# Optimization experiments

Measured on AMD Instinct MI355X. Metric: run time of the kernel, lower is better.

The kernel has to match this reference:

```python
import jax, jax.numpy as jnp
import numpy as np

# GPT-2 decoder (mlm=False path of the Keras GPT module), no past/KV-cache,
# no explicit mask -> causal mask, dropout disabled (training=False).
N_HEAD = 12
NINF = -10000.0  # Attention.ninf
EPS = 1e-6


def layer_norm(x, g, b):
    m = jnp.mean(x, axis=-1, keepdims=True)
    v = jnp.mean(jnp.square(x - m), axis=-1, keepdims=True)
    return (x - m) / jnp.sqrt(v + EPS) * g + b


def gelu(x):
    # 0.5*x*(1+erf(x/sqrt(2))) as in gelu_activating
    return 0.5 * x * (1.0 + jax.lax.erf(x * np.float32(1.0 / np.sqrt(2.0))))


def setup_inputs() -> dict:
    key = jax.random.key(0)
    B, S, D, L, V, CTX = 4, 512, 768, 12, 50257, 1024
    F = 4 * D
    ks = jax.random.split(key, 10)
    init = lambda k, shape: (jax.random.normal(k, shape, jnp.float32) * 0.02)
    return {
        "x": jax.random.randint(ks[0], (B, S), 0, V),
        "emb": init(ks[1], (V, D)),        # wte (tied output projection)
        "posemb": init(ks[2], (CTX, D)),   # wpe
        "ln1_g": jnp.ones((L, D)), "ln1_b": jnp.zeros((L, D)),
        "wqkv": init(ks[3], (L, D, 3 * D)), "bqkv": jnp.zeros((L, 3 * D)),
        "wo": init(ks[4], (L, D, D)), "bo": jnp.zeros((L, D)),
        "ln2_g": jnp.ones((L, D)), "ln2_b": jnp.zeros((L, D)),
        "wfc": init(ks[5], (L, D, F)), "bfc": jnp.zeros((L, F)),
        "wproj": init(ks[6], (L, F, D)), "bproj": jnp.zeros((L, D)),
        "lnf_g": jnp.ones((D,)), "lnf_b": jnp.zeros((D,)),
    }


def reference(x, emb, posemb, ln1_g, ln1_b, wqkv, bqkv, wo, bo,
              ln2_g, ln2_b, wfc, bfc, wproj, bproj, lnf_g, lnf_b):
    B, S = x.shape
    L, D, _ = wqkv.shape
    H = N_HEAD
    hd = D // H
    scale = np.float32(1.0 / np.sqrt(hd))

    # Embedding (mlm=False): token + positional, no layernorm
    h = emb[x] + posemb[:S]  # [B,S,D]

    # causal mask: positions j > i get NINF (m1 = range(q)[:,None] < range(k)-k+q)
    mask = (jnp.arange(S)[:, None] < jnp.arange(S)[None, :]).astype(jnp.float32) * NINF

    for i in range(L):
        # pre-norm attention
        qkv = layer_norm(h, ln1_g[i], ln1_b[i]) @ wqkv[i] + bqkv[i]  # [B,S,3D]
        q, k, v = jnp.split(qkv, 3, axis=-1)
        q = q.reshape(B, S, H, hd).transpose(0, 2, 1, 3)  # [B,H,S,hd]
        k = k.reshape(B, S, H, hd).transpose(0, 2, 1, 3)
        v = v.reshape(B, S, H, hd).transpose(0, 2, 1, 3)
        scores = jnp.einsum('bhqd,bhkd->bhqk', q, k) * scale + mask
        a = jax.nn.softmax(scores, axis=-1)  # [B,H,S,S]
        o = jnp.einsum('bhqk,bhkd->bhqd', a, v)
        o = o.transpose(0, 2, 1, 3).reshape(B, S, D)
        h = h + (o @ wo[i] + bo[i])  # residual
        # pre-norm MLP
        m = layer_norm(h, ln2_g[i], ln2_b[i])
        h = h + (gelu(m @ wfc[i] + bfc[i]) @ wproj[i] + bproj[i])

    hidden = layer_norm(h, lnf_g, lnf_b)          # model/lnorm_f
    logits = hidden @ emb.T                        # tied embedding projection
    probs = jax.nn.softmax(logits, axis=-1)        # softmax=True
    return (probs, hidden)
```

## Files before the change

kernel.cpp:

```cpp
#include <hip/hip_runtime.h>
#include <hip/hip_bf16.h>

typedef __bf16 bf16_t;
typedef bf16_t bf16x8 __attribute__((ext_vector_type(8)));
typedef float  f32x4  __attribute__((ext_vector_type(4)));

__device__ __forceinline__ void gload16(const void* g, void* l) {
    __builtin_amdgcn_global_load_lds(
        (const __attribute__((address_space(1))) unsigned int*)g,
        (__attribute__((address_space(3))) unsigned int*)l, 16, 0, 0);
}

__device__ __forceinline__ void drain_and_barrier() {
    __builtin_amdgcn_sched_barrier(0);
    asm volatile("s_waitcnt vmcnt(0)" ::: "memory");
    __builtin_amdgcn_s_barrier();
    __builtin_amdgcn_sched_barrier(0);
}

__global__ void embed_kernel(const int* __restrict__ x,
                             const float* __restrict__ emb,
                             const float* __restrict__ pos,
                             float* __restrict__ h,
                             int S, int D, int total)
{
    int i = blockIdx.x * blockDim.x + threadIdx.x;
    if (i >= total) return;
    int d  = i % D;
    int bs = i / D;
    int s  = bs % S;
    h[i] = emb[(long long)x[bs] * D + d] + pos[(long long)s * D + d];
}

__global__ void convert_bf16(const float* __restrict__ in, bf16_t* __restrict__ out, int n4)
{
    int i = blockIdx.x * blockDim.x + threadIdx.x;
    for (; i < n4; i += gridDim.x * blockDim.x) {
        float4 v = ((const float4*)in)[i];
        bf16_t* o = out + (size_t)i * 4;
        o[0] = (bf16_t)v.x; o[1] = (bf16_t)v.y; o[2] = (bf16_t)v.z; o[3] = (bf16_t)v.w;
    }
}

__global__ __launch_bounds__(256) void transpose_to_bf16(
    const float* __restrict__ in, bf16_t* __restrict__ out, int K, int N)
{
    const float* ip = in  + (size_t)blockIdx.z * K * N;
    bf16_t*      op = out + (size_t)blockIdx.z * K * N;
    __shared__ float t[32][33];
    const int n0 = blockIdx.x * 32, k0 = blockIdx.y * 32;
    const int tx = threadIdx.x, ty = threadIdx.y;
#pragma unroll
    for (int u = 0; u < 4; ++u)
        t[ty + u * 8][tx] = ip[(size_t)(k0 + ty + u * 8) * N + (n0 + tx)];
    __syncthreads();
#pragma unroll
    for (int u = 0; u < 4; ++u)
        op[(size_t)(n0 + ty + u * 8) * K + (k0 + tx)] = (bf16_t)t[tx][ty + u * 8];
}

__global__ __launch_bounds__(256) void transpose_v(
    const bf16_t* __restrict__ qkv, bf16_t* __restrict__ vT)
{
    constexpr int S = 512, TD = 2304, D = 768, H = 12;
    const int z = blockIdx.y, bb = z / H, hh = z - bb * H;
    const int k0 = blockIdx.x * 64;
    const bf16_t* src = qkv + (size_t)(bb * S + k0) * TD + 2 * D + hh * 64;
    bf16_t* dst = vT + (size_t)z * 64 * S + k0;
    __shared__ bf16_t sm[64][68];
    const int c = threadIdx.x & 63, rq = threadIdx.x >> 6;
#pragma unroll
    for (int u = 0; u < 16; ++u) {
        const int r = u * 4 + rq;
        sm[r][c] = src[(size_t)r * TD + c];
    }
    __syncthreads();
#pragma unroll
    for (int u = 0; u < 16; ++u) {
        const int d = u * 4 + rq;
        dst[(size_t)d * S + c] = sm[c][d];
    }
}

__global__ __launch_bounds__(256) void layernorm_dual(
    const float* __restrict__ X, const float* __restrict__ g,
    const float* __restrict__ b, bf16_t* __restrict__ Yb,
    float* __restrict__ Yf, int D)
{
    const int row = blockIdx.x;
    const float* xr = X + (long long)row * D;
    const int tid = threadIdx.x;

    float vals[3];
    float s = 0.0f;
#pragma unroll
    for (int u = 0; u < 3; ++u) { vals[u] = xr[tid + u * 256]; s += vals[u]; }

    __shared__ float red[256];
    red[tid] = s;
    __syncthreads();
    for (int off = 128; off > 0; off >>= 1) {
        if (tid < off) red[tid] += red[tid + off];
        __syncthreads();
    }
    const float mean = red[0] / (float)D;
    __syncthreads();

    float vs = 0.0f;
#pragma unroll
    for (int u = 0; u < 3; ++u) { float d = vals[u] - mean; vs += d * d; }
    red[tid] = vs;
    __syncthreads();
    for (int off = 128; off > 0; off >>= 1) {
        if (tid < off) red[tid] += red[tid + off];
        __syncthreads();
    }
    const float var  = red[0] / (float)D;
    const float rstd = rsqrtf(var + 1e-6f);

#pragma unroll
    for (int u = 0; u < 3; ++u) {
        const int c = tid + u * 256;
        const float y = (vals[u] - mean) * rstd * g[c] + b[c];
        Yb[(long long)row * D + c] = (bf16_t)y;
        if (Yf) Yf[(long long)row * D + c] = y;
    }
}

__global__ __launch_bounds__(256) void flash_attn(
    const bf16_t* __restrict__ qkv, const bf16_t* __restrict__ vT,
    bf16_t* __restrict__ o)
{
    constexpr int S = 512, TD = 2304, D = 768, H = 12;
    const int qt = blockIdx.x;
    const int z  = blockIdx.y;
    const int bb = z / H, hh = z - bb * H;
    const int tid = threadIdx.x, lane = tid & 63, w = tid >> 6;
    const int fr = lane & 15, g = lane >> 4, sub = g * 8;

    __shared__ bf16_t kS[2][4096];
    __shared__ bf16_t vS[2][4096];
    __shared__ bf16_t pS[4][32 * 72];

    bf16x8 qf[2][2];
    const bf16_t* qbase = qkv + (size_t)(bb * S + qt * 128 + w * 32) * TD + hh * 64;
#pragma unroll
    for (int m = 0; m < 2; ++m)
#pragma unroll
        for (int ks = 0; ks < 2; ++ks) {
            bf16x8 v = *(const bf16x8*)&qbase[(size_t)(m * 16 + fr) * TD + ks * 32 + sub];
#pragma unroll
            for (int j = 0; j < 8; ++j) v[j] = v[j] * (bf16_t)0.125f;
            qf[m][ks] = v;
        }

    f32x4 oacc[2][4];
    float mrun[2][4], lrun[2][4];
#pragma unroll
    for (int m = 0; m < 2; ++m)
#pragma unroll
        for (int r = 0; r < 4; ++r) { mrun[m][r] = -3.0e38f; lrun[m][r] = 0.0f; }
#pragma unroll
    for (int m = 0; m < 2; ++m)
#pragma unroll
        for (int n = 0; n < 4; ++n)
            oacc[m][n] = (f32x4){0.f, 0.f, 0.f, 0.f};

    int qr[2][4];
#pragma unroll
    for (int m = 0; m < 2; ++m)
#pragma unroll
        for (int r = 0; r < 4; ++r)
            qr[m][r] = qt * 128 + w * 32 + m * 16 + g * 4 + r;

    const int srow8  = lane >> 3;
    const int schunk = (lane & 7) ^ (srow8 & 7);

    const bf16_t* kGbase = qkv + (size_t)(bb * S) * TD + D + hh * 64;
    const bf16_t* vGbase = vT + (size_t)z * 64 * S;
    const int nkv = 2 * qt + 2;

#define STAGE_KV(buf, t)                                                        \
    {                                                                           \
        _Pragma("unroll")                                                       \
        for (int it = 0; it < 2; ++it) {                                        \
            const int row = it * 32 + w * 8 + srow8;                            \
            gload16(kGbase + (size_t)((t) * 64 + row) * TD + schunk * 8,        \
                    &kS[buf][it * 2048 + w * 512]);                             \
            gload16(vGbase + (size_t)row * S + (t) * 64 + schunk * 8,           \
                    &vS[buf][it * 2048 + w * 512]);                             \
        }                                                                       \
    }

    STAGE_KV(0, 0);
    drain_and_barrier();

    int cur = 0;
    for (int t = 0; t < nkv; ++t) {
        if (t + 1 < nkv) STAGE_KV(cur ^ 1, t + 1);

        f32x4 sacc[2][4];
#pragma unroll
        for (int m = 0; m < 2; ++m)
#pragma unroll
            for (int n = 0; n < 4; ++n)
                sacc[m][n] = (f32x4){0.f, 0.f, 0.f, 0.f};
#pragma unroll
        for (int ks = 0; ks < 2; ++ks) {
            bf16x8 bK[4];
#pragma unroll
            for (int n = 0; n < 4; ++n) {
                const int rw = n * 16 + fr;
                const int c  = ks * 4 + g;
                bK[n] = *(const bf16x8*)&kS[cur][rw * 64 + ((c ^ (rw & 7)) << 3)];
            }
#pragma unroll
            for (int m = 0; m < 2; ++m)
#pragma unroll
                for (int n = 0; n < 4; ++n)
                    sacc[m][n] = __builtin_amdgcn_mfma_f32_16x16x32_bf16(
                        qf[m][ks], bK[n], sacc[m][n], 0, 0, 0);
        }

        if (t >= 2 * qt) {
#pragma unroll
            for (int m = 0; m < 2; ++m)
#pragma unroll
                for (int n = 0; n < 4; ++n) {
                    const int key = t * 64 + n * 16 + fr;
#pragma unroll
                    for (int r = 0; r < 4; ++r)
                        if (key > qr[m][r]) sacc[m][n][r] = -3.0e38f;
                }
        }

        float sf[2][4], rs[2][4];
#pragma unroll
        for (int m = 0; m < 2; ++m)
#pragma unroll
            for (int r = 0; r < 4; ++r) {
                float v = fmaxf(fmaxf(sacc[m][0][r], sacc[m][1][r]),
                                fmaxf(sacc[m][2][r], sacc[m][3][r]));
#pragma unroll
                for (int off = 1; off < 16; off <<= 1)
                    v = fmaxf(v, __shfl_xor(v, off));
                const float mn = fmaxf(mrun[m][r], v);
                sf[m][r] = __expf(mrun[m][r] - mn);
                mrun[m][r] = mn;
                lrun[m][r] *= sf[m][r];
            }
#pragma unroll
        for (int m = 0; m < 2; ++m)
#pragma unroll
            for (int n = 0; n < 4; ++n)
#pragma unroll
                for (int r = 0; r < 4; ++r)
                    oacc[m][n][r] *= sf[m][r];
#pragma unroll
        for (int m = 0; m < 2; ++m)
#pragma unroll
            for (int r = 0; r < 4; ++r) rs[m][r] = 0.0f;
#pragma unroll
        for (int m = 0; m < 2; ++m)
#pragma unroll
            for (int n = 0; n < 4; ++n)
#pragma unroll
                for (int r = 0; r < 4; ++r) {
                    const float p = __expf(sacc[m][n][r] - mrun[m][r]);
                    sacc[m][n][r] = p;
                    rs[m][r] += p;
                }
#pragma unroll
        for (int m = 0; m < 2; ++m)
#pragma unroll
            for (int r = 0; r < 4; ++r) {
                float v = rs[m][r];
#pragma unroll
                for (int off = 1; off < 16; off <<= 1) v += __shfl_xor(v, off);
                lrun[m][r] += v;
            }

        bf16_t* pw = pS[w];
#pragma unroll
        for (int m = 0; m < 2; ++m)
#pragma unroll
            for (int n = 0; n < 4; ++n)
#pragma unroll
                for (int r = 0; r < 4; ++r)
                    pw[(m * 16 + g * 4 + r) * 72 + n * 16 + fr] = (bf16_t)sacc[m][n][r];

#pragma unroll
        for (int ks = 0; ks < 2; ++ks) {
            bf16x8 pa[2], vb[4];
#pragma unroll
            for (int m = 0; m < 2; ++m)
                pa[m] = *(const bf16x8*)&pw[(m * 16 + fr) * 72 + ks * 32 + sub];
#pragma unroll
            for (int n = 0; n < 4; ++n) {
                const int rw = n * 16 + fr;
                const int c  = ks * 4 + g;
                vb[n] = *(const bf16x8*)&vS[cur][rw * 64 + ((c ^ (rw & 7)) << 3)];
            }
#pragma unroll
            for (int m = 0; m < 2; ++m)
#pragma unroll
                for (int n = 0; n < 4; ++n)
                    oacc[m][n] = __builtin_amdgcn_mfma_f32_16x16x32_bf16(
                        pa[m], vb[n], oacc[m][n], 0, 0, 0);
        }
        drain_and_barrier();
        cur ^= 1;
    }
#undef STAGE_KV

    bf16_t* obase = o + (size_t)(bb * S + qt * 128 + w * 32) * D + hh * 64;
#pragma unroll
    for (int m = 0; m < 2; ++m)
#pragma unroll
        for (int r = 0; r < 4; ++r) {
            const float inv = 1.0f / lrun[m][r];
#pragma unroll
            for (int n = 0; n < 4; ++n)
                obase[(size_t)(m * 16 + g * 4 + r) * D + n * 16 + fr] =
                    (bf16_t)(oacc[m][n][r] * inv);
        }
}

__global__ __launch_bounds__(256) void softmax_vocab(
    const bf16_t* __restrict__ logits, float* __restrict__ probs, int V, int Vp)
{
    const int tid = threadIdx.x;
    const bf16_t* lr = logits + (size_t)blockIdx.x * Vp;
    float* pr = probs + (size_t)blockIdx.x * V;
    const int n8 = V >> 3;

    float m = -3.0e38f, s = 0.0f;
    for (int c8 = tid; c8 < n8; c8 += 256) {
        const bf16x8 v = *(const bf16x8*)(lr + (size_t)c8 * 8);
        float f[8], lm = -3.0e38f;
#pragma unroll
        for (int j = 0; j < 8; ++j) { f[j] = (float)v[j]; lm = fmaxf(lm, f[j]); }
        if (lm > m) { s *= __expf(m - lm); m = lm; }
#pragma unroll
        for (int j = 0; j < 8; ++j) s += __expf(f[j] - m);
    }
    for (int c = n8 * 8 + tid; c < V; c += 256) {
        const float f = (float)lr[c];
        if (f > m) { s *= __expf(m - f); m = f; }
        s += __expf(f - m);
    }

    __shared__ float mS[256], sS[256];
    mS[tid] = m; sS[tid] = s;
    __syncthreads();
    for (int off = 128; off > 0; off >>= 1) {
        if (tid < off) {
            const float m1 = mS[tid], m2 = mS[tid + off];
            const float M_ = fmaxf(m1, m2);
            sS[tid] = sS[tid] * __expf(m1 - M_) + sS[tid + off] * __expf(m2 - M_);
            mS[tid] = M_;
        }
        __syncthreads();
    }
    const float M_  = mS[0];
    const float inv = 1.0f / sS[0];

    for (int c8 = tid; c8 < n8; c8 += 256) {
        const bf16x8 v = *(const bf16x8*)(lr + (size_t)c8 * 8);
#pragma unroll
        for (int j = 0; j < 8; ++j)
            pr[(size_t)c8 * 8 + j] = __expf((float)v[j] - M_) * inv;
    }
    for (int c = n8 * 8 + tid; c < V; c += 256)
        pr[c] = __expf((float)lr[c] - M_) * inv;
}

template<bool ADD, bool GELU_, bool OUTBF, bool DB, bool HALFN>
__device__ __forceinline__ void gemm_body(
    const bf16_t* __restrict__ A, const bf16_t* __restrict__ Bw,
    const float* __restrict__ bias, void* __restrict__ Cv,
    int M, int N, int K, int lda, int ldb, int ldc)
{
    constexpr int BN  = HALFN ? 64 : 128;
    constexpr int BUF = HALFN ? 12288 : 16384;
    __shared__ bf16_t lds[(DB ? 2 : 1) * BUF];

    const int tid  = threadIdx.x;
    const int lane = tid & 63;
    const int w    = tid >> 6;
    const int row0 = blockIdx.x * 128;
    const int col0 = blockIdx.y * BN;

    const int row8 = lane >> 3;
    const int sch  = (lane & 7) ^ row8;
    const int fr   = lane & 15;
    const int g    = lane >> 4;

    const int aRowB = row0 + w * 32;
    const int bRowB = HALFN ? (col0 + w * 16) : (col0 + w * 32);

    constexpr int MR = HALFN ? 2 : 4;
    const int wr = HALFN ? w : (w >> 1);
    const int wc = HALFN ? 0 : (w & 1);

    f32x4 acc[MR][4];
#pragma unroll
    for (int m = 0; m < MR; ++m)
#pragma unroll
        for (int n = 0; n < 4; ++n)
            acc[m][n] = (f32x4){0.f, 0.f, 0.f, 0.f};

    auto STAGE = [&](int buf, int k0) {
        bf16_t* lb = lds + buf * BUF;
#pragma unroll
        for (int it = 0; it < 4; ++it) {
            const int ar = aRowB + it * 8 + row8;
            gload16(A + (size_t)ar * lda + k0 + sch * 8, lb + w * 2048 + it * 512);
        }
#pragma unroll
        for (int it = 0; it < (HALFN ? 2 : 4); ++it) {
            int br = bRowB + it * 8 + row8;
            if (br >= N) br = 0;
            gload16(Bw + (size_t)br * ldb + k0 + sch * 8,
                    lb + 8192 + w * (HALFN ? 1024 : 2048) + it * 512);
        }
    };

    auto COMPUTE = [&](int buf) {
        bf16_t* lb = lds + buf * BUF;
#pragma unroll
        for (int ks = 0; ks < 2; ++ks) {
            bf16x8 af[MR], bfr[4];
            const int cs = ks * 4 + g;
#pragma unroll
            for (int m = 0; m < MR; ++m) {
                const int row = (HALFN ? w * 32 : wr * 64) + m * 16 + fr;
                af[m] = *(const bf16x8*)&lb[row * 64 + ((cs ^ (fr & 7)) << 3)];
            }
#pragma unroll
            for (int n = 0; n < 4; ++n) {
                const int row = (HALFN ? 0 : wc * 64) + n * 16 + fr;
                bfr[n] = *(const bf16x8*)&lb[8192 + row * 64 + ((cs ^ (fr & 7)) << 3)];
            }
#pragma unroll
            for (int m = 0; m < MR; ++m)
#pragma unroll
                for (int n = 0; n < 4; ++n)
                    acc[m][n] = __builtin_amdgcn_mfma_f32_16x16x32_bf16(
                        af[m], bfr[n], acc[m][n], 0, 0, 0);
        }
    };

    const int nt = K >> 6;
    if (DB) {
        STAGE(0, 0);
        drain_and_barrier();
        int cur = 0;
        for (int t = 0; t < nt; ++t) {
            if (t + 1 < nt) STAGE(cur ^ 1, (t + 1) << 6);
            COMPUTE(cur);
            drain_and_barrier();
            cur ^= 1;
        }
    } else {
        for (int t = 0; t < nt; ++t) {
            STAGE(0, t << 6);
            __syncthreads();
            COMPUTE(0);
            __syncthreads();
        }
    }

    const int rBase = row0 + (HALFN ? w * 32 : wr * 64) + g * 4;
    const int cBase = col0 + (HALFN ? 0 : wc * 64) + fr;
    float bv[4];
#pragma unroll
    for (int n = 0; n < 4; ++n) {
        const int c = cBase + n * 16;
        bv[n] = (bias && c < N) ? bias[c] : 0.0f;
    }
#pragma unroll
    for (int m = 0; m < MR; ++m) {
#pragma unroll
        for (int r = 0; r < 4; ++r) {
            const int rr = rBase + m * 16 + r;
#pragma unroll
            for (int n = 0; n < 4; ++n) {
                const int c = cBase + n * 16;
                if (c >= N) continue;
                float v = acc[m][n][r] + bv[n];
                if (GELU_) v = 0.5f * v * (1.0f + erff(v * 0.70710678118654752f));
                if (OUTBF) {
                    ((bf16_t*)Cv)[(size_t)rr * ldc + c] = (bf16_t)v;
                } else {
                    float* Cf = (float*)Cv;
                    const size_t idx = (size_t)rr * ldc + c;
                    if (ADD) v += Cf[idx];
                    Cf[idx] = v;
                }
            }
        }
    }
}

__global__ __launch_bounds__(256) void k_gemm_qkv(
    const bf16_t* A, const bf16_t* B, const float* bias, void* C,
    int M, int N, int K, int lda, int ldb, int ldc)
{ gemm_body<false, false, true, true, true>(A, B, bias, C, M, N, K, lda, ldb, ldc); }

__global__ __launch_bounds__(256) void k_gemm_oproj(
    const bf16_t* A, const bf16_t* B, const float* bias, void* C,
    int M, int N, int K, int lda, int ldb, int ldc)
{ gemm_body<true, false, false, true, true>(A, B, bias, C, M, N, K, lda, ldb, ldc); }

__global__ __launch_bounds__(256) void k_gemm_fc(
    const bf16_t* A, const bf16_t* B, const float* bias, void* C,
    int M, int N, int K, int lda, int ldb, int ldc)
{ gemm_body<false, true, true, true, true>(A, B, bias, C, M, N, K, lda, ldb, ldc); }

__global__ __launch_bounds__(256) void k_gemm_proj(
    const bf16_t* A, const bf16_t* B, const float* bias, void* C,
    int M, int N, int K, int lda, int ldb, int ldc)
{ gemm_body<true, false, false, true, true>(A, B, bias, C, M, N, K, lda, ldb, ldc); }

__global__ __launch_bounds__(256) void k_gemm_head(
    const bf16_t* __restrict__ A, const bf16_t* __restrict__ Bw,
    bf16_t* __restrict__ C, int M, int N, int K, int lda, int ldb, int ldc)
{
    __shared__ bf16_t lds[24576];

    const int tid  = threadIdx.x;
    const int lane = tid & 63;
    const int w    = tid >> 6;
    const int wr   = w >> 1, wc = w & 1;
    const int row0 = blockIdx.x * 128;
    const int col0 = blockIdx.y * 256;

    const int row8 = lane >> 3;
    const int sch  = (lane & 7) ^ row8;
    const int fr   = lane & 15;
    const int g    = lane >> 4;

    const int aRowB = row0 + w * 32;
    const int bRowB = col0 + w * 64;

    f32x4 acc[4][8];
#pragma unroll
    for (int m = 0; m < 4; ++m)
#pragma unroll
        for (int n = 0; n < 8; ++n)
            acc[m][n] = (f32x4){0.f, 0.f, 0.f, 0.f};

    for (int k0 = 0; k0 < K; k0 += 64) {
#pragma unroll
        for (int it = 0; it < 4; ++it) {
            const int ar = aRowB + it * 8 + row8;
            gload16(A + (size_t)ar * lda + k0 + sch * 8, lds + w * 2048 + it * 512);
        }
#pragma unroll
        for (int it = 0; it < 8; ++it) {
            int br = bRowB + it * 8 + row8;
            if (br >= N) br = 0;
            gload16(Bw + (size_t)br * ldb + k0 + sch * 8,
                    lds + 8192 + w * 4096 + it * 512);
        }
        __syncthreads();

#pragma unroll
        for (int ks = 0; ks < 2; ++ks) {
            const int cs = ks * 4 + g;
            bf16x8 af[4];
#pragma unroll
            for (int m = 0; m < 4; ++m) {
                const int row = wr * 64 + m * 16 + fr;
                af[m] = *(const bf16x8*)&lds[row * 64 + ((cs ^ (fr & 7)) << 3)];
            }
#pragma unroll
            for (int hf = 0; hf < 2; ++hf) {
                bf16x8 bfr[4];
#pragma unroll
                for (int n = 0; n < 4; ++n) {
                    const int row = hf * 128 + wc * 64 + n * 16 + fr;
                    bfr[n] = *(const bf16x8*)&lds[8192 + row * 64 + ((cs ^ (fr & 7)) << 3)];
                }
#pragma unroll
                for (int m = 0; m < 4; ++m)
#pragma unroll
                    for (int n = 0; n < 4; ++n)
                        acc[m][hf * 4 + n] = __builtin_amdgcn_mfma_f32_16x16x32_bf16(
                            af[m], bfr[n], acc[m][hf * 4 + n], 0, 0, 0);
            }
        }
        __syncthreads();
    }

    const int rBase = row0 + wr * 64 + g * 4;
#pragma unroll
    for (int m = 0; m < 4; ++m) {
#pragma unroll
        for (int r = 0; r < 4; ++r) {
            const int rr = rBase + m * 16 + r;
#pragma unroll
            for (int hf = 0; hf < 2; ++hf) {
#pragma unroll
                for (int n = 0; n < 4; ++n) {
                    const int c = col0 + hf * 128 + wc * 64 + n * 16 + fr;
                    if (c < N)
                        C[(size_t)rr * ldc + c] = (bf16_t)acc[m][hf * 4 + n][r];
                }
            }
        }
    }
}

extern "C" void kernel_launch(void* const* d_in, const int* in_sizes, int n_in,
                              void* d_out, int out_size, void* d_ws, size_t ws_size,
                              hipStream_t stream)
{
    constexpr int B = 4, S = 512, D = 768, L = 12, V = 50257, H = 12, F = 3072;
    constexpr int M  = B * S;
    constexpr int TD = 3 * D;
    constexpr int BH = B * H;
    constexpr int Vp = 50264;

    const int*   x    = (const int*)  d_in[0];
    const float* emb  = (const float*)d_in[1];
    const float* pos  = (const float*)d_in[2];
    const float* ln1g = (const float*)d_in[3];
    const float* ln1b = (const float*)d_in[4];
    const float* wqkv = (const float*)d_in[5];
    const float* bqkv = (const float*)d_in[6];
    const float* wo   = (const float*)d_in[7];
    const float* bo   = (const float*)d_in[8];
    const float* ln2g = (const float*)d_in[9];
    const float* ln2b = (const float*)d_in[10];
    const float* wfc  = (const float*)d_in[11];
    const float* bfc  = (const float*)d_in[12];
    const float* wpr  = (const float*)d_in[13];
    const float* bpr  = (const float*)d_in[14];
    const float* lnfg = (const float*)d_in[15];
    const float* lnfb = (const float*)d_in[16];

    float* probs  = (float*)d_out;
    float* hidden = probs + (size_t)M * V;

    float*  h      = (float*)d_ws;
    bf16_t* qkv_bf = (bf16_t*)(h + (size_t)M * D);
    bf16_t* vT     = qkv_bf + (size_t)M * TD;
    bf16_t* xn_bf  = vT     + (size_t)BH * 64 * S;
    bf16_t* o_bf   = xn_bf  + (size_t)M * D;
    bf16_t* mid_bf = o_bf   + (size_t)M * D;
    bf16_t* wqkvT  = mid_bf + (size_t)M * F;
    bf16_t* woT    = wqkvT  + (size_t)L * D * TD;
    bf16_t* wfcT   = woT    + (size_t)L * D * D;
    bf16_t* wprT   = wfcT   + (size_t)L * D * F;
    bf16_t* hid_bf = wprT   + (size_t)L * F * D;
    bf16_t* embB   = hid_bf + (size_t)M * D;
    bf16_t* logits = (bf16_t*)d_ws;

    convert_bf16<<<2048, 256, 0, stream>>>(emb, embB, (V * D) / 4);
    transpose_to_bf16<<<dim3(TD / 32, D / 32, L), dim3(32, 8), 0, stream>>>(wqkv, wqkvT, D, TD);
    transpose_to_bf16<<<dim3(D / 32,  D / 32, L), dim3(32, 8), 0, stream>>>(wo,   woT,   D, D);
    transpose_to_bf16<<<dim3(F / 32,  D / 32, L), dim3(32, 8), 0, stream>>>(wfc,  wfcT,  D, F);
    transpose_to_bf16<<<dim3(D / 32,  F / 32, L), dim3(32, 8), 0, stream>>>(wpr,  wprT,  F, D);

    embed_kernel<<<dim3((M * D + 255) / 256), 256, 0, stream>>>(x, emb, pos, h, S, D, M * D);

    for (int i = 0; i < L; ++i) {
        layernorm_dual<<<M, 256, 0, stream>>>(h, ln1g + (size_t)i * D, ln1b + (size_t)i * D,
                                              xn_bf, nullptr, D);

        k_gemm_qkv<<<dim3(M / 128, TD / 64), 256, 0, stream>>>(
            xn_bf, wqkvT + (size_t)i * D * TD, bqkv + (size_t)i * TD, qkv_bf,
            M, TD, D, D, D, TD);

        transpose_v<<<dim3(S / 64, BH), 256, 0, stream>>>(qkv_bf, vT);

        flash_attn<<<dim3(S / 128, BH), 256, 0, stream>>>(qkv_bf, vT, o_bf);

        k_gemm_oproj<<<dim3(M / 128, D / 64), 256, 0, stream>>>(
            o_bf, woT + (size_t)i * D * D, bo + (size_t)i * D, h,
            M, D, D, D, D, D);

        layernorm_dual<<<M, 256, 0, stream>>>(h, ln2g + (size_t)i * D, ln2b + (size_t)i * D,
                                              xn_bf, nullptr, D);

        k_gemm_fc<<<dim3(M / 128, F / 64), 256, 0, stream>>>(
            xn_bf, wfcT + (size_t)i * D * F, bfc + (size_t)i * F, mid_bf,
            M, F, D, D, D, F);

        k_gemm_proj<<<dim3(M / 128, D / 64), 256, 0, stream>>>(
            mid_bf, wprT + (size_t)i * F * D, bpr + (size_t)i * D, h,
            M, D, F, F, F, D);
    }

    layernorm_dual<<<M, 256, 0, stream>>>(h, lnfg, lnfb, hid_bf, hidden, D);

    k_gemm_head<<<dim3(M / 128, (V + 255) / 256), 256, 0, stream>>>(
        hid_bf, embB, logits,
        M, V, D, D, D, Vp);

    softmax_vocab<<<M, 256, 0, stream>>>(logits, probs, V, Vp);
}
```

Before: 2.370 ms.

## Fuse V transpose into flash attention and shrink head GEMM tile

Removes the separate transpose_v kernel. Flash attention now loads V rows from the qkv buffer into registers and scatters them transposed into swizzled LDS, with the global loads overlapping the current tile's compute. Separately, the vocab head GEMM tile is narrowed from 128x256 to 128x128, which halves the accumulators and LDS per block and launches twice as many blocks. This trades one kernel launch and a global round trip for scalar LDS stores in attention, and gives the head GEMM lower per-block reuse in exchange for higher occupancy.

```diff
diff --git a/kernel.cpp b/kernel.cpp
--- a/kernel.cpp
+++ b/kernel.cpp
@@ -59,29 +59,6 @@
         op[(size_t)(n0 + ty + u * 8) * K + (k0 + tx)] = (bf16_t)t[tx][ty + u * 8];
 }
 
-__global__ __launch_bounds__(256) void transpose_v(
-    const bf16_t* __restrict__ qkv, bf16_t* __restrict__ vT)
-{
-    constexpr int S = 512, TD = 2304, D = 768, H = 12;
-    const int z = blockIdx.y, bb = z / H, hh = z - bb * H;
-    const int k0 = blockIdx.x * 64;
-    const bf16_t* src = qkv + (size_t)(bb * S + k0) * TD + 2 * D + hh * 64;
-    bf16_t* dst = vT + (size_t)z * 64 * S + k0;
-    __shared__ bf16_t sm[64][68];
-    const int c = threadIdx.x & 63, rq = threadIdx.x >> 6;
-#pragma unroll
-    for (int u = 0; u < 16; ++u) {
-        const int r = u * 4 + rq;
-        sm[r][c] = src[(size_t)r * TD + c];
-    }
-    __syncthreads();
-#pragma unroll
-    for (int u = 0; u < 16; ++u) {
-        const int d = u * 4 + rq;
-        dst[(size_t)d * S + c] = sm[c][d];
-    }
-}
-
 __global__ __launch_bounds__(256) void layernorm_dual(
     const float* __restrict__ X, const float* __restrict__ g,
     const float* __restrict__ b, bf16_t* __restrict__ Yb,
@@ -128,8 +105,7 @@
 }
 
 __global__ __launch_bounds__(256) void flash_attn(
-    const bf16_t* __restrict__ qkv, const bf16_t* __restrict__ vT,
-    bf16_t* __restrict__ o)
+    const bf16_t* __restrict__ qkv, bf16_t* __restrict__ o)
 {
     constexpr int S = 512, TD = 2304, D = 768, H = 12;
     const int qt = blockIdx.x;
@@ -177,27 +153,45 @@
     const int schunk = (lane & 7) ^ (srow8 & 7);
 
     const bf16_t* kGbase = qkv + (size_t)(bb * S) * TD + D + hh * 64;
-    const bf16_t* vGbase = vT + (size_t)z * 64 * S;
+    const bf16_t* vGbase = qkv + (size_t)(bb * S) * TD + 2 * D + hh * 64;
     const int nkv = 2 * qt + 2;
 
-#define STAGE_KV(buf, t)                                                        \
+    bf16x8 vreg[2];
+
+#define STAGE_ISSUE(buf, t)                                                     \
     {                                                                           \
         _Pragma("unroll")                                                       \
         for (int it = 0; it < 2; ++it) {                                        \
             const int row = it * 32 + w * 8 + srow8;                            \
             gload16(kGbase + (size_t)((t) * 64 + row) * TD + schunk * 8,        \
                     &kS[buf][it * 2048 + w * 512]);                             \
-            gload16(vGbase + (size_t)row * S + (t) * 64 + schunk * 8,           \
-                    &vS[buf][it * 2048 + w * 512]);                             \
         }                                                                       \
-    }
-
-    STAGE_KV(0, 0);
-    drain_and_barrier();
+        _Pragma("unroll")                                                       \
+        for (int it = 0; it < 2; ++it) {                                        \
+            const int dch = w * 2 + it;                                         \
+            vreg[it] = *(const bf16x8*)&vGbase[(size_t)((t) * 64 + lane) * TD + dch * 8]; \
+        }                                                                       \
+    }
+#define STAGE_WRITE(buf)                                                        \
+    {                                                                           \
+        _Pragma("unroll")                                                       \
+        for (int it = 0; it < 2; ++it) {                                        \
+            const int dch = w * 2 + it;                                         \
+            _Pragma("unroll")                                                   \
+            for (int j = 0; j < 8; ++j) {                                       \
+                const int d = dch * 8 + j;                                      \
+                vS[buf][d * 64 + (((lane >> 3) ^ j) << 3) + (lane & 7)] = vreg[it][j]; \
+            }                                                                   \
+        }                                                                       \
+    }
+
+    STAGE_ISSUE(0, 0);
+    STAGE_WRITE(0);
+    __syncthreads();
 
     int cur = 0;
     for (int t = 0; t < nkv; ++t) {
-        if (t + 1 < nkv) STAGE_KV(cur ^ 1, t + 1);
+        if (t + 1 < nkv) STAGE_ISSUE(cur ^ 1, t + 1);
 
         f32x4 sacc[2][4];
 #pragma unroll
@@ -308,10 +302,13 @@
                     oacc[m][n] = __builtin_amdgcn_mfma_f32_16x16x32_bf16(
                         pa[m], vb[n], oacc[m][n], 0, 0, 0);
         }
-        drain_and_barrier();
+
+        if (t + 1 < nkv) STAGE_WRITE(cur ^ 1);
+        __syncthreads();
         cur ^= 1;
     }
-#undef STAGE_KV
+#undef STAGE_ISSUE
+#undef STAGE_WRITE
 
     bf16_t* obase = o + (size_t)(bb * S + qt * 128 + w * 32) * D + hh * 64;
 #pragma unroll
@@ -527,14 +524,14 @@
     const bf16_t* __restrict__ A, const bf16_t* __restrict__ Bw,
     bf16_t* __restrict__ C, int M, int N, int K, int lda, int ldb, int ldc)
 {
-    __shared__ bf16_t lds[24576];
+    __shared__ bf16_t lds[16384];
 
     const int tid  = threadIdx.x;
     const int lane = tid & 63;
     const int w    = tid >> 6;
     const int wr   = w >> 1, wc = w & 1;
     const int row0 = blockIdx.x * 128;
-    const int col0 = blockIdx.y * 256;
+    const int col0 = blockIdx.y * 128;
 
     const int row8 = lane >> 3;
     const int sch  = (lane & 7) ^ row8;
@@ -542,74 +539,63 @@
     const int g    = lane >> 4;
 
     const int aRowB = row0 + w * 32;
-    const int bRowB = col0 + w * 64;
-
-    f32x4 acc[4][8];
+    const int bRowB = col0 + w * 32;
+
+    f32x4 acc[4][4];
 #pragma unroll
     for (int m = 0; m < 4; ++m)
 #pragma unroll
-        for (int n = 0; n < 8; ++n)
+        for (int n = 0; n < 4; ++n)
             acc[m][n] = (f32x4){0.f, 0.f, 0.f, 0.f};
 
     for (int k0 = 0; k0 < K; k0 += 64) {
 #pragma unroll
         for (int it = 0; it < 4; ++it) {
             const int ar = aRowB + it * 8 + row8;
-            gload16(A + (size_t)ar * lda + k0 + sch * 8, lds + w * 2048 + it * 512);
-        }
-#pragma unroll
-        for (int it = 0; it < 8; ++it) {
+            gload16(A + (size_t)ar * lda + k0 + sch * 8,
+                    lds + w * 2048 + it * 512);
             int br = bRowB + it * 8 + row8;
             if (br >= N) br = 0;
             gload16(Bw + (size_t)br * ldb + k0 + sch * 8,
-                    lds + 8192 + w * 4096 + it * 512);
+                    lds + 8192 + w * 2048 + it * 512);
         }
         __syncthreads();
 
 #pragma unroll
         for (int ks = 0; ks < 2; ++ks) {
+            bf16x8 af[4], bfr[4];
             const int cs = ks * 4 + g;
-            bf16x8 af[4];
 #pragma unroll
             for (int m = 0; m < 4; ++m) {
                 const int row = wr * 64 + m * 16 + fr;
                 af[m] = *(const bf16x8*)&lds[row * 64 + ((cs ^ (fr & 7)) << 3)];
             }
 #pragma unroll
-            for (int hf = 0; hf < 2; ++hf) {
-                bf16x8 bfr[4];
-#pragma unroll
-                for (int n = 0; n < 4; ++n) {
-                    const int row = hf * 128 + wc * 64 + n * 16 + fr;
-                    bfr[n] = *(const bf16x8*)&lds[8192 + row * 64 + ((cs ^ (fr & 7)) << 3)];
-                }
-#pragma unroll
-                for (int m = 0; m < 4; ++m)
-#pragma unroll
-                    for (int n = 0; n < 4; ++n)
-                        acc[m][hf * 4 + n] = __builtin_amdgcn_mfma_f32_16x16x32_bf16(
-                            af[m], bfr[n], acc[m][hf * 4 + n], 0, 0, 0);
-            }
+            for (int n = 0; n < 4; ++n) {
+                const int row = wc * 64 + n * 16 + fr;
+                bfr[n] = *(const bf16x8*)&lds[8192 + row * 64 + ((cs ^ (fr & 7)) << 3)];
+            }
+#pragma unroll
+            for (int m = 0; m < 4; ++m)
+#pragma unroll
+                for (int n = 0; n < 4; ++n)
+                    acc[m][n] = __builtin_amdgcn_mfma_f32_16x16x32_bf16(
+                        af[m], bfr[n], acc[m][n], 0, 0, 0);
         }
         __syncthreads();
     }
 
     const int rBase = row0 + wr * 64 + g * 4;
-#pragma unroll
-    for (int m = 0; m < 4; ++m) {
-#pragma unroll
-        for (int r = 0; r < 4; ++r) {
-            const int rr = rBase + m * 16 + r;
-#pragma unroll
-            for (int hf = 0; hf < 2; ++hf) {
-#pragma unroll
-                for (int n = 0; n < 4; ++n) {
-                    const int c = col0 + hf * 128 + wc * 64 + n * 16 + fr;
-                    if (c < N)
-                        C[(size_t)rr * ldc + c] = (bf16_t)acc[m][hf * 4 + n][r];
-                }
-            }
-        }
+    const int cBase = col0 + wc * 64 + fr;
+#pragma unroll
+    for (int n = 0; n < 4; ++n) {
+        const int c = cBase + n * 16;
+        if (c >= N) continue;
+#pragma unroll
+        for (int m = 0; m < 4; ++m)
+#pragma unroll
+            for (int r = 0; r < 4; ++r)
+                C[(size_t)(rBase + m * 16 + r) * ldc + c] = (bf16_t)acc[m][n][r];
     }
 }
 
@@ -646,8 +632,7 @@
 
     float*  h      = (float*)d_ws;
     bf16_t* qkv_bf = (bf16_t*)(h + (size_t)M * D);
-    bf16_t* vT     = qkv_bf + (size_t)M * TD;
-    bf16_t* xn_bf  = vT     + (size_t)BH * 64 * S;
+    bf16_t* xn_bf  = qkv_bf + (size_t)M * TD;
     bf16_t* o_bf   = xn_bf  + (size_t)M * D;
     bf16_t* mid_bf = o_bf   + (size_t)M * D;
     bf16_t* wqkvT  = mid_bf + (size_t)M * F;
@@ -674,9 +659,7 @@
             xn_bf, wqkvT + (size_t)i * D * TD, bqkv + (size_t)i * TD, qkv_bf,
             M, TD, D, D, D, TD);
 
-        transpose_v<<<dim3(S / 64, BH), 256, 0, stream>>>(qkv_bf, vT);
-
-        flash_attn<<<dim3(S / 128, BH), 256, 0, stream>>>(qkv_bf, vT, o_bf);
+        flash_attn<<<dim3(S / 128, BH), 256, 0, stream>>>(qkv_bf, o_bf);
 
         k_gemm_oproj<<<dim3(M / 128, D / 64), 256, 0, stream>>>(
             o_bf, woT + (size_t)i * D * D, bo + (size_t)i * D, h,
@@ -696,7 +679,7 @@
 
     layernorm_dual<<<M, 256, 0, stream>>>(h, lnfg, lnfb, hid_bf, hidden, D);
 
-    k_gemm_head<<<dim3(M / 128, (V + 255) / 256), 256, 0, stream>>>(
+    k_gemm_head<<<dim3(M / 128, (V + 127) / 128), 256, 0, stream>>>(
         hid_bf, embB, logits,
         M, V, D, D, D, Vp);
 
```

Result: faster. 2.164 ms (-8.7%).
